# Kernel optimization log

Hardware: AMD Instinct MI355X
Metric: run time of the kernel (lower is better)

Reference implementation:

```python
import jax, jax.numpy as jnp
import numpy as np

MAX_IT = 20
LAMBDA_ROF = 7.0
SIGMA = 1.0 / (7.0 * 0.01)
TAU = 0.01
THETA = 0.5

H, W_DIM = 4096, 4096


def forward_weighted_gradient(x, w):
    # x: (1,H,W), w: (2,H,W) -> (2,H,W)
    x0 = x[0]
    gh = jnp.pad(x0[:, 1:] - x0[:, :-1], ((0, 0), (0, 1)))   # grad[0,:, :-1]
    gv = jnp.pad(x0[1:, :] - x0[:-1, :], ((0, 1), (0, 0)))   # grad[1,:-1,:]
    return jnp.stack([gh, gv], axis=0) * w


def backward_divergence(y):
    # y: (2,H,W) -> (1,H,W)
    yh, yv = y[0], y[1]
    d_h = jnp.concatenate(
        [yh[:, :1], yh[:, 1:-1] - yh[:, :-2], -yh[:, -2:-1]], axis=1)
    d_v = jnp.concatenate(
        [yv[:1, :], yv[1:-1, :] - yv[:-2, :], -yv[-2:-1, :]], axis=0)
    return (d_h + d_v)[None]


def prox_linf_ball(p, r):
    # p - detach(max(p-r,0) - max(-p-r,0))  (clamp treated as data in torch code)
    shrink = jnp.maximum(p - r, 0.0) - jnp.maximum(-p - r, 0.0)
    return p - jax.lax.stop_gradient(shrink)


def setup_inputs() -> dict:
    key = jax.random.key(0)
    k1, _ = jax.random.split(key)
    img_obs = jax.random.uniform(k1, (1, H, W_DIM), dtype=jnp.float32)
    w = jnp.ones((2, H, W_DIM), dtype=jnp.float32)
    return {"img_obs": img_obs, "w": w}


def reference(img_obs, w):
    x0 = img_obs
    x_tilde0 = img_obs
    y0 = jnp.zeros((2,) + img_obs.shape[1:], dtype=img_obs.dtype)

    def step(carry, _):
        x, x_tilde, y = carry
        y = y + SIGMA * forward_weighted_gradient(x_tilde, w)
        y = prox_linf_ball(y, 1.0)
        x_old = x
        x = (x + TAU * backward_divergence(y)
             + LAMBDA_ROF * TAU * img_obs) / (1.0 + LAMBDA_ROF * TAU)
        x_tilde = x + THETA * (x - x_old)
        return (x, x_tilde, y), None

    (x, x_tilde, y), _ = jax.lax.scan(step, (x0, x_tilde0, y0), None, length=MAX_IT)
    return x_tilde
```

## Files before the change

kernel.cpp:

```cpp
#include <hip/hip_runtime.h>

static constexpr int H = 4096;
static constexpr int W = 4096;
static constexpr long N = (long)H * W;

static constexpr int TILE = 64;
static constexpr int HOFF = 12;
static constexpr int R    = TILE + 2*HOFF;
static constexpr int S    = R;
static constexpr int PS   = R * S;
static constexpr int CPR  = R / 8;
static constexpr int NCH  = R * CPR;
static constexpr int NT   = 512;

static constexpr float SIGMA = 14.285714285714286f;
static constexpr float INVD  = 1.0f / 1.07f;
static constexpr float TIV   = 0.01f / 1.07f;
static constexpr float CF    = 0.07f / 1.07f;

typedef _Float16 half8  __attribute__((ext_vector_type(8)));
typedef _Float16 half4v __attribute__((ext_vector_type(4)));

__device__ __forceinline__ half8 splat8(float f) {
    _Float16 h = (_Float16)f;
    half8 v = {h, h, h, h, h, h, h, h};
    return v;
}
__device__ __forceinline__ half8 clamp8(half8 v) {
    v = __builtin_elementwise_min(v, splat8(1.0f));
    v = __builtin_elementwise_max(v, splat8(-1.0f));
    return v;
}

__global__ __launch_bounds__(256) void pack_w(
    const float* __restrict__ wg, _Float16* __restrict__ whp, _Float16* __restrict__ wvp)
{
    const long p = ((long)blockIdx.x * 256 + threadIdx.x) * 8;
    const int i = (int)(p >> 12);
    const float4* hp = reinterpret_cast<const float4*>(wg + p);
    float4 a = hp[0], b = hp[1];
    const float4* vp = reinterpret_cast<const float4*>(wg + N + p);
    float4 c = vp[0], d = vp[1];
    half8 wh, wv;
    wh[0]=(_Float16)(SIGMA*a.x); wh[1]=(_Float16)(SIGMA*a.y);
    wh[2]=(_Float16)(SIGMA*a.z); wh[3]=(_Float16)(SIGMA*a.w);
    wh[4]=(_Float16)(SIGMA*b.x); wh[5]=(_Float16)(SIGMA*b.y);
    wh[6]=(_Float16)(SIGMA*b.z); wh[7]=(_Float16)(SIGMA*b.w);
    wv[0]=(_Float16)(SIGMA*c.x); wv[1]=(_Float16)(SIGMA*c.y);
    wv[2]=(_Float16)(SIGMA*c.z); wv[3]=(_Float16)(SIGMA*c.w);
    wv[4]=(_Float16)(SIGMA*d.x); wv[5]=(_Float16)(SIGMA*d.y);
    wv[6]=(_Float16)(SIGMA*d.z); wv[7]=(_Float16)(SIGMA*d.w);
    if ((p & 4095) + 8 == W) wh[7] = (_Float16)0.0f;
    if (i == H - 1) wv = splat8(0.0f);
    *reinterpret_cast<half8*>(whp + p) = wh;
    *reinterpret_cast<half8*>(wvp + p) = wv;
}

template<int PHASE>
__global__ __launch_bounds__(NT, 4) void fused_pd(
    const float* __restrict__ img,
    const _Float16* __restrict__ whp, const _Float16* __restrict__ wvp,
    _Float16* __restrict__ xg, _Float16* __restrict__ yhg, _Float16* __restrict__ yvg,
    float* __restrict__ out)
{
    __shared__ _Float16 lds_s[2 * PS + NCH + 2];
    _Float16* __restrict__ xtp = lds_s;
    _Float16* __restrict__ yvp = lds_s + PS;
    _Float16* __restrict__ yhe = lds_s + 2 * PS;

    const int tid = threadIdx.x;
    const int gi0 = blockIdx.y * TILE - HOFF;
    const int gj0 = blockIdx.x * TILE - HOFF;
    const bool interior = (gi0 >= 0) && (gj0 >= 0) && (gi0 + R <= H) && (gj0 + R <= W);

    const int t0 = tid, t1 = tid + NT;
    const int i0_ = t0 / CPR, i1_ = t1 / CPR;
    const int b0 = i0_ * S + (t0 - i0_ * CPR) * 8;
    const int b1 = i1_ * S + (t1 - i1_ * CPR) * 8;
    const bool act1 = (t1 < NCH);

    const half8 kTIV  = splat8(TIV);
    const half8 kINVD = splat8(INVD);
    const half8 k15   = splat8(1.5f);
    const half8 kM05  = splat8(-0.5f);

    half8 wh0, wh1, wv0, wv1;
    half8 ci0, ci1;
    half8 x0, x1;
    half8 xt0r, xt1r;
    half8 yh0, yh1, yv0, yv1;

    auto loadC = [&](int t, half8& whr, half8& wvr, half8& cir, half8& xr,
                     half8& xtr, half8& yhr, half8& yvr) {
        const int i  = t / CPR;
        const int j0 = (t - i * CPR) * 8;
        const int gi = gi0 + i;
        const int gj = gj0 + j0;
        if (interior) {
            const long o = (long)gi * W + gj;
            const float4* ip = reinterpret_cast<const float4*>(img + o);
            float4 a = ip[0], b = ip[1];
            float im[8] = {a.x, a.y, a.z, a.w, b.x, b.y, b.z, b.w};
            whr = *reinterpret_cast<const half8*>(whp + o);
            wvr = *reinterpret_cast<const half8*>(wvp + o);
#pragma unroll
            for (int k = 0; k < 8; ++k) cir[k] = (_Float16)(CF * im[k]);
            if (PHASE == 0) {
#pragma unroll
                for (int k = 0; k < 8; ++k) xr[k] = (_Float16)im[k];
                xtr = xr;
                yhr = splat8(0.f); yvr = splat8(0.f);
            } else {
                xr  = *reinterpret_cast<const half8*>(xg  + o);
                yhr = *reinterpret_cast<const half8*>(yhg + o);
                yvr = *reinterpret_cast<const half8*>(yvg + o);
            }
        } else {
            const int gic = min(max(gi, 0), H - 1);
            const bool rowin = (gi >= 0) && (gi < H);
#pragma unroll
            for (int k = 0; k < 8; ++k) {
                const int gjk = gj + k;
                const int gjc = min(max(gjk, 0), W - 1);
                const bool inim = rowin && (gjk >= 0) && (gjk < W);
                const long o = (long)gic * W + gjc;
                const float imf = img[o];
                whr[k] = inim ? whp[o] : (_Float16)0.0f;
                wvr[k] = inim ? wvp[o] : (_Float16)0.0f;
                cir[k] = (_Float16)(CF * imf);
                if (PHASE == 0) {
                    xr[k]  = (_Float16)imf;
                    xtr[k] = (_Float16)imf;
                    yhr[k] = (_Float16)0.0f;
                    yvr[k] = (_Float16)0.0f;
                } else {
                    xr[k]  = xg[o];
                    yhr[k] = inim ? yhg[o] : (_Float16)0.0f;
                    yvr[k] = inim ? yvg[o] : (_Float16)0.0f;
                }
            }
        }
        const int base = i * S + j0;
        if (PHASE == 0) {
            *reinterpret_cast<half8*>(xtp + base) = xtr;
        } else {
            *reinterpret_cast<half8*>(xtp + base) = xr;
            *reinterpret_cast<half8*>(yvp + base) = yvr;
            yhe[t + 1] = yhr[7];
        }
    };
    loadC(t0, wh0, wv0, ci0, x0, xt0r, yh0, yv0);
    if (act1) loadC(t1, wh1, wv1, ci1, x1, xt1r, yh1, yv1);
    if (tid == 0) yhe[0] = (_Float16)0.0f;
    __syncthreads();

    auto dual_all = [&](bool write_yhe) {
        _Float16 rt0 = xtp[b0 + 8];
        half8 bv0 = *reinterpret_cast<const half8*>(xtp + b0 + S);
        _Float16 rt1 = (_Float16)0.f; half8 bv1;
        if (act1) {
            rt1 = xtp[b1 + 8];
            bv1 = *reinterpret_cast<const half8*>(xtp + b1 + S);
        }
        {
            half8 sh = __builtin_shufflevector(xt0r, xt0r, 1, 2, 3, 4, 5, 6, 7, 7);
            sh[7] = rt0;
            yh0 = clamp8((sh - xt0r) * wh0 + yh0);
            yv0 = clamp8((bv0 - xt0r) * wv0 + yv0);
            *reinterpret_cast<half8*>(yvp + b0) = yv0;
            if (write_yhe) yhe[t0 + 1] = yh0[7];
        }
        if (act1) {
            half8 sh = __builtin_shufflevector(xt1r, xt1r, 1, 2, 3, 4, 5, 6, 7, 7);
            sh[7] = rt1;
            yh1 = clamp8((sh - xt1r) * wh1 + yh1);
            yv1 = clamp8((bv1 - xt1r) * wv1 + yv1);
            *reinterpret_cast<half8*>(yvp + b1) = yv1;
            if (write_yhe) yhe[t1 + 1] = yh1[7];
        }
    };
    auto prim_all = [&]() {
        _Float16 yl0 = yhe[t0];
        half8 yva0 = *reinterpret_cast<const half8*>(yvp + b0 - S);
        _Float16 yl1 = (_Float16)0.f; half8 yva1;
        if (act1) {
            yl1  = yhe[t1];
            yva1 = *reinterpret_cast<const half8*>(yvp + b1 - S);
        }
        {
            half8 ysh = __builtin_shufflevector(yh0, yh0, 0, 0, 1, 2, 3, 4, 5, 6);
            ysh[0] = yl0;
            half8 dv = (yh0 - ysh) + (yv0 - yva0);
            half8 tt = dv * kTIV + ci0;
            half8 xn = x0 * kINVD + tt;
            half8 xt = xn * k15 + x0 * kM05;
            x0 = xn; xt0r = xt;
            *reinterpret_cast<half8*>(xtp + b0) = xt;
        }
        if (act1) {
            half8 ysh = __builtin_shufflevector(yh1, yh1, 0, 0, 1, 2, 3, 4, 5, 6);
            ysh[0] = yl1;
            half8 dv = (yh1 - ysh) + (yv1 - yva1);
            half8 tt = dv * kTIV + ci1;
            half8 xn = x1 * kINVD + tt;
            half8 xt = xn * k15 + x1 * kM05;
            x1 = xn; xt1r = xt;
            *reinterpret_cast<half8*>(xtp + b1) = xt;
        }
    };

    if (PHASE == 1) {
        prim_all();
        __syncthreads();
    }
    const int NIT = (PHASE == 0) ? 10 : 9;
    for (int it = 0; it < NIT; ++it) {
        dual_all(true);
        __syncthreads();
        prim_all();
        __syncthreads();
    }
    if (PHASE == 0) {
        dual_all(false);
        __syncthreads();
    }

    const int r  = tid >> 3;
    const int k  = tid & 7;
    const int lb = (HOFF + r) * S + HOFF + k * 8;
    const long gb = (long)(blockIdx.y * TILE + r) * W + blockIdx.x * TILE + k * 8;

    if (PHASE == 0) {
        {
            half4v a0 = *reinterpret_cast<const half4v*>(yvp + lb);
            half4v a1 = *reinterpret_cast<const half4v*>(yvp + lb + 4);
            half8 o; o[0]=a0[0];o[1]=a0[1];o[2]=a0[2];o[3]=a0[3];
                     o[4]=a1[0];o[5]=a1[1];o[6]=a1[2];o[7]=a1[3];
            *reinterpret_cast<half8*>(yvg + gb) = o;
        }
        __syncthreads();
        *reinterpret_cast<half8*>(xtp + b0) = x0;
        *reinterpret_cast<half8*>(yvp + b0) = yh0;
        if (act1) {
            *reinterpret_cast<half8*>(xtp + b1) = x1;
            *reinterpret_cast<half8*>(yvp + b1) = yh1;
        }
        __syncthreads();
        {
            half4v a0 = *reinterpret_cast<const half4v*>(xtp + lb);
            half4v a1 = *reinterpret_cast<const half4v*>(xtp + lb + 4);
            half8 o; o[0]=a0[0];o[1]=a0[1];o[2]=a0[2];o[3]=a0[3];
                     o[4]=a1[0];o[5]=a1[1];o[6]=a1[2];o[7]=a1[3];
            *reinterpret_cast<half8*>(xg + gb) = o;
            half4v b0v = *reinterpret_cast<const half4v*>(yvp + lb);
            half4v b1v = *reinterpret_cast<const half4v*>(yvp + lb + 4);
            half8 o2; o2[0]=b0v[0];o2[1]=b0v[1];o2[2]=b0v[2];o2[3]=b0v[3];
                      o2[4]=b1v[0];o2[5]=b1v[1];o2[6]=b1v[2];o2[7]=b1v[3];
            *reinterpret_cast<half8*>(yhg + gb) = o2;
        }
    } else {
        half4v a = *reinterpret_cast<const half4v*>(xtp + lb);
        half4v b = *reinterpret_cast<const half4v*>(xtp + lb + 4);
        float4 o0 = make_float4((float)a[0], (float)a[1], (float)a[2], (float)a[3]);
        float4 o1 = make_float4((float)b[0], (float)b[1], (float)b[2], (float)b[3]);
        *reinterpret_cast<float4*>(out + gb)     = o0;
        *reinterpret_cast<float4*>(out + gb + 4) = o1;
    }
}

extern "C" void kernel_launch(void* const* d_in, const int* in_sizes, int n_in,
                              void* d_out, int out_size, void* d_ws, size_t ws_size,
                              hipStream_t stream) {
    const float* img = (const float*)d_in[0];
    const float* wg  = (const float*)d_in[1];
    float* out = (float*)d_out;

    _Float16* ws16 = (_Float16*)d_ws;
    _Float16* whp = ws16;
    _Float16* wvp = ws16 + N;
    _Float16* xg  = ws16 + 2 * N;
    _Float16* yhg = ws16 + 3 * N;
    _Float16* yvg = ws16 + 4 * N;

    pack_w<<<dim3((int)(N / 8 / 256)), dim3(256), 0, stream>>>(wg, whp, wvp);

    dim3 grid(W / TILE, H / TILE);
    fused_pd<0><<<grid, dim3(NT), 0, stream>>>(img, whp, wvp, xg, yhg, yvg, out);
    fused_pd<1><<<grid, dim3(NT), 0, stream>>>(img, whp, wvp, xg, yhg, yvg, out);
}
```

Baseline: 344.6 us.

## Pair rows per thread so vertical neighbours come from registers, shrinking LDS traffic

Each thread now owns two vertically adjacent 8-wide chunks (rows 2p and 2p+1) instead of two chunks far apart. The vertical gradient and divergence between the paired rows are taken directly from registers. Only the even-row xt, odd-row yv, and single boundary halves go through LDS, which halves the shared-memory arrays and the LDS reads and writes per iteration. Final results are written straight from registers to global memory, dropping the extra LDS staging passes and barriers. The cost is more complex indexing, partial-vector edge stores, and some idle threads, since only NTASK of the 512 threads are active.

```diff
diff --git a/kernel.cpp b/kernel.cpp
--- a/kernel.cpp
+++ b/kernel.cpp
@@ -7,10 +7,10 @@
 static constexpr int TILE = 64;
 static constexpr int HOFF = 12;
 static constexpr int R    = TILE + 2*HOFF;
-static constexpr int S    = R;
-static constexpr int PS   = R * S;
 static constexpr int CPR  = R / 8;
-static constexpr int NCH  = R * CPR;
+static constexpr int PR   = R / 2;
+static constexpr int NTASK= PR * CPR;
+static constexpr int PSE  = PR * R;
 static constexpr int NT   = 512;
 
 static constexpr float SIGMA = 14.285714285714286f;
@@ -30,6 +30,12 @@
     v = __builtin_elementwise_min(v, splat8(1.0f));
     v = __builtin_elementwise_max(v, splat8(-1.0f));
     return v;
+}
+__device__ __forceinline__ half4v lo4(half8 v) {
+    half4v r = {v[0], v[1], v[2], v[3]}; return r;
+}
+__device__ __forceinline__ half4v hi4(half8 v) {
+    half4v r = {v[4], v[5], v[6], v[7]}; return r;
 }
 
 __global__ __launch_bounds__(256) void pack_w(
@@ -63,21 +69,22 @@
     _Float16* __restrict__ xg, _Float16* __restrict__ yhg, _Float16* __restrict__ yvg,
     float* __restrict__ out)
 {
-    __shared__ _Float16 lds_s[2 * PS + NCH + 2];
-    _Float16* __restrict__ xtp = lds_s;
-    _Float16* __restrict__ yvp = lds_s + PS;
-    _Float16* __restrict__ yhe = lds_s + 2 * PS;
+    __shared__ _Float16 lds_s[2 * PSE + 3 * (NTASK + 2)];
+    _Float16* __restrict__ xte  = lds_s;
+    _Float16* __restrict__ yvo  = lds_s + PSE;
+    _Float16* __restrict__ yheA = lds_s + 2 * PSE;
+    _Float16* __restrict__ yheB = yheA + (NTASK + 2);
+    _Float16* __restrict__ xteo = yheB + (NTASK + 2);
 
     const int tid = threadIdx.x;
+    const bool act = tid < NTASK;
+    const int t  = act ? tid : 0;
+    const int p  = t / CPR;
+    const int j0 = (t - p * CPR) * 8;
+    const int be = p * R + j0;
     const int gi0 = blockIdx.y * TILE - HOFF;
     const int gj0 = blockIdx.x * TILE - HOFF;
     const bool interior = (gi0 >= 0) && (gj0 >= 0) && (gi0 + R <= H) && (gj0 + R <= W);
-
-    const int t0 = tid, t1 = tid + NT;
-    const int i0_ = t0 / CPR, i1_ = t1 / CPR;
-    const int b0 = i0_ * S + (t0 - i0_ * CPR) * 8;
-    const int b1 = i1_ * S + (t1 - i1_ * CPR) * 8;
-    const bool act1 = (t1 < NCH);
 
     const half8 kTIV  = splat8(TIV);
     const half8 kINVD = splat8(INVD);
@@ -90,12 +97,8 @@
     half8 xt0r, xt1r;
     half8 yh0, yh1, yv0, yv1;
 
-    auto loadC = [&](int t, half8& whr, half8& wvr, half8& cir, half8& xr,
-                     half8& xtr, half8& yhr, half8& yvr) {
-        const int i  = t / CPR;
-        const int j0 = (t - i * CPR) * 8;
-        const int gi = gi0 + i;
-        const int gj = gj0 + j0;
+    auto loadRow = [&](int gi, int gj, half8& whr, half8& wvr, half8& cir,
+                       half8& xr, half8& yhr, half8& yvr) {
         if (interior) {
             const long o = (long)gi * W + gj;
             const float4* ip = reinterpret_cast<const float4*>(img + o);
@@ -108,7 +111,6 @@
             if (PHASE == 0) {
 #pragma unroll
                 for (int k = 0; k < 8; ++k) xr[k] = (_Float16)im[k];
-                xtr = xr;
                 yhr = splat8(0.f); yvr = splat8(0.f);
             } else {
                 xr  = *reinterpret_cast<const half8*>(xg  + o);
@@ -130,7 +132,6 @@
                 cir[k] = (_Float16)(CF * imf);
                 if (PHASE == 0) {
                     xr[k]  = (_Float16)imf;
-                    xtr[k] = (_Float16)imf;
                     yhr[k] = (_Float16)0.0f;
                     yvr[k] = (_Float16)0.0f;
                 } else {
@@ -140,131 +141,138 @@
                 }
             }
         }
-        const int base = i * S + j0;
+    };
+    if (act) {
+        const int gi = gi0 + 2 * p;
+        const int gj = gj0 + j0;
+        loadRow(gi,     gj, wh0, wv0, ci0, x0, yh0, yv0);
+        loadRow(gi + 1, gj, wh1, wv1, ci1, x1, yh1, yv1);
         if (PHASE == 0) {
-            *reinterpret_cast<half8*>(xtp + base) = xtr;
+            xt0r = x0; xt1r = x1;
+            *reinterpret_cast<half8*>(xte + be) = xt0r;
+            *reinterpret_cast<half8*>(yvo + be) = splat8(0.f);
+            xteo[t] = xt1r[0];
+            yheA[1 + t] = (_Float16)0.0f;
+            yheB[1 + t] = (_Float16)0.0f;
         } else {
-            *reinterpret_cast<half8*>(xtp + base) = xr;
-            *reinterpret_cast<half8*>(yvp + base) = yvr;
-            yhe[t + 1] = yhr[7];
+            *reinterpret_cast<half8*>(yvo + be) = yv1;
+            yheA[1 + t] = yh0[7];
+            yheB[1 + t] = yh1[7];
+        }
+    }
+    if (tid == NT - 1) {
+        yheA[0] = (_Float16)0.0f;
+        yheB[0] = (_Float16)0.0f;
+        xteo[NTASK]     = (_Float16)0.0f;
+        xteo[NTASK + 1] = (_Float16)0.0f;
+    }
+    __syncthreads();
+
+    auto dual_all = [&](bool writes) {
+        if (act) {
+            _Float16 rt0 = xte[be + 8];
+            _Float16 rt1 = xteo[t + 1];
+            half8 bv1 = *reinterpret_cast<const half8*>(xte + be + R);
+            half8 sh0 = __builtin_shufflevector(xt0r, xt0r, 1, 2, 3, 4, 5, 6, 7, 7);
+            sh0[7] = rt0;
+            half8 sh1 = __builtin_shufflevector(xt1r, xt1r, 1, 2, 3, 4, 5, 6, 7, 7);
+            sh1[7] = rt1;
+            yh0 = clamp8((sh0 - xt0r) * wh0 + yh0);
+            yv0 = clamp8((xt1r - xt0r) * wv0 + yv0);
+            yh1 = clamp8((sh1 - xt1r) * wh1 + yh1);
+            yv1 = clamp8((bv1 - xt1r) * wv1 + yv1);
+            if (writes) {
+                *reinterpret_cast<half8*>(yvo + be) = yv1;
+                yheA[1 + t] = yh0[7];
+                yheB[1 + t] = yh1[7];
+            }
         }
     };
-    loadC(t0, wh0, wv0, ci0, x0, xt0r, yh0, yv0);
-    if (act1) loadC(t1, wh1, wv1, ci1, x1, xt1r, yh1, yv1);
-    if (tid == 0) yhe[0] = (_Float16)0.0f;
-    __syncthreads();
-
-    auto dual_all = [&](bool write_yhe) {
-        _Float16 rt0 = xtp[b0 + 8];
-        half8 bv0 = *reinterpret_cast<const half8*>(xtp + b0 + S);
-        _Float16 rt1 = (_Float16)0.f; half8 bv1;
-        if (act1) {
-            rt1 = xtp[b1 + 8];
-            bv1 = *reinterpret_cast<const half8*>(xtp + b1 + S);
-        }
-        {
-            half8 sh = __builtin_shufflevector(xt0r, xt0r, 1, 2, 3, 4, 5, 6, 7, 7);
-            sh[7] = rt0;
-            yh0 = clamp8((sh - xt0r) * wh0 + yh0);
-            yv0 = clamp8((bv0 - xt0r) * wv0 + yv0);
-            *reinterpret_cast<half8*>(yvp + b0) = yv0;
-            if (write_yhe) yhe[t0 + 1] = yh0[7];
-        }
-        if (act1) {
-            half8 sh = __builtin_shufflevector(xt1r, xt1r, 1, 2, 3, 4, 5, 6, 7, 7);
-            sh[7] = rt1;
-            yh1 = clamp8((sh - xt1r) * wh1 + yh1);
-            yv1 = clamp8((bv1 - xt1r) * wv1 + yv1);
-            *reinterpret_cast<half8*>(yvp + b1) = yv1;
-            if (write_yhe) yhe[t1 + 1] = yh1[7];
+    auto prim_all = [&](bool writes) {
+        if (act) {
+            _Float16 yl0 = yheA[t];
+            _Float16 yl1 = yheB[t];
+            half8 yva0 = *reinterpret_cast<const half8*>(yvo + be - R);
+            half8 ysh0 = __builtin_shufflevector(yh0, yh0, 0, 0, 1, 2, 3, 4, 5, 6);
+            ysh0[0] = yl0;
+            half8 ysh1 = __builtin_shufflevector(yh1, yh1, 0, 0, 1, 2, 3, 4, 5, 6);
+            ysh1[0] = yl1;
+            half8 dv0 = (yh0 - ysh0) + (yv0 - yva0);
+            half8 dv1 = (yh1 - ysh1) + (yv1 - yv0);
+            half8 tt0 = dv0 * kTIV + ci0;
+            half8 xn0 = x0 * kINVD + tt0;
+            half8 xtn0 = xn0 * k15 + x0 * kM05;
+            x0 = xn0; xt0r = xtn0;
+            half8 tt1 = dv1 * kTIV + ci1;
+            half8 xn1 = x1 * kINVD + tt1;
+            half8 xtn1 = xn1 * k15 + x1 * kM05;
+            x1 = xn1; xt1r = xtn1;
+            if (writes) {
+                *reinterpret_cast<half8*>(xte + be) = xt0r;
+                xteo[t] = xt1r[0];
+            }
         }
     };
-    auto prim_all = [&]() {
-        _Float16 yl0 = yhe[t0];
-        half8 yva0 = *reinterpret_cast<const half8*>(yvp + b0 - S);
-        _Float16 yl1 = (_Float16)0.f; half8 yva1;
-        if (act1) {
-            yl1  = yhe[t1];
-            yva1 = *reinterpret_cast<const half8*>(yvp + b1 - S);
-        }
-        {
-            half8 ysh = __builtin_shufflevector(yh0, yh0, 0, 0, 1, 2, 3, 4, 5, 6);
-            ysh[0] = yl0;
-            half8 dv = (yh0 - ysh) + (yv0 - yva0);
-            half8 tt = dv * kTIV + ci0;
-            half8 xn = x0 * kINVD + tt;
-            half8 xt = xn * k15 + x0 * kM05;
-            x0 = xn; xt0r = xt;
-            *reinterpret_cast<half8*>(xtp + b0) = xt;
-        }
-        if (act1) {
-            half8 ysh = __builtin_shufflevector(yh1, yh1, 0, 0, 1, 2, 3, 4, 5, 6);
-            ysh[0] = yl1;
-            half8 dv = (yh1 - ysh) + (yv1 - yva1);
-            half8 tt = dv * kTIV + ci1;
-            half8 xn = x1 * kINVD + tt;
-            half8 xt = xn * k15 + x1 * kM05;
-            x1 = xn; xt1r = xt;
-            *reinterpret_cast<half8*>(xtp + b1) = xt;
-        }
-    };
 
     if (PHASE == 1) {
-        prim_all();
+        prim_all(true);
         __syncthreads();
     }
     const int NIT = (PHASE == 0) ? 10 : 9;
     for (int it = 0; it < NIT; ++it) {
         dual_all(true);
         __syncthreads();
-        prim_all();
+        prim_all(!(PHASE == 1 && it == NIT - 1));
         __syncthreads();
     }
     if (PHASE == 0) {
         dual_all(false);
-        __syncthreads();
-    }
-
-    const int r  = tid >> 3;
-    const int k  = tid & 7;
-    const int lb = (HOFF + r) * S + HOFF + k * 8;
-    const long gb = (long)(blockIdx.y * TILE + r) * W + blockIdx.x * TILE + k * 8;
-
-    if (PHASE == 0) {
-        {
-            half4v a0 = *reinterpret_cast<const half4v*>(yvp + lb);
-            half4v a1 = *reinterpret_cast<const half4v*>(yvp + lb + 4);
-            half8 o; o[0]=a0[0];o[1]=a0[1];o[2]=a0[2];o[3]=a0[3];
-                     o[4]=a1[0];o[5]=a1[1];o[6]=a1[2];o[7]=a1[3];
-            *reinterpret_cast<half8*>(yvg + gb) = o;
-        }
-        __syncthreads();
-        *reinterpret_cast<half8*>(xtp + b0) = x0;
-        *reinterpret_cast<half8*>(yvp + b0) = yh0;
-        if (act1) {
-            *reinterpret_cast<half8*>(xtp + b1) = x1;
-            *reinterpret_cast<half8*>(yvp + b1) = yh1;
-        }
-        __syncthreads();
-        {
-            half4v a0 = *reinterpret_cast<const half4v*>(xtp + lb);
-            half4v a1 = *reinterpret_cast<const half4v*>(xtp + lb + 4);
-            half8 o; o[0]=a0[0];o[1]=a0[1];o[2]=a0[2];o[3]=a0[3];
-                     o[4]=a1[0];o[5]=a1[1];o[6]=a1[2];o[7]=a1[3];
-            *reinterpret_cast<half8*>(xg + gb) = o;
-            half4v b0v = *reinterpret_cast<const half4v*>(yvp + lb);
-            half4v b1v = *reinterpret_cast<const half4v*>(yvp + lb + 4);
-            half8 o2; o2[0]=b0v[0];o2[1]=b0v[1];o2[2]=b0v[2];o2[3]=b0v[3];
-                      o2[4]=b1v[0];o2[5]=b1v[1];o2[6]=b1v[2];o2[7]=b1v[3];
-            *reinterpret_cast<half8*>(yhg + gb) = o2;
-        }
-    } else {
-        half4v a = *reinterpret_cast<const half4v*>(xtp + lb);
-        half4v b = *reinterpret_cast<const half4v*>(xtp + lb + 4);
-        float4 o0 = make_float4((float)a[0], (float)a[1], (float)a[2], (float)a[3]);
-        float4 o1 = make_float4((float)b[0], (float)b[1], (float)b[2], (float)b[3]);
-        *reinterpret_cast<float4*>(out + gb)     = o0;
-        *reinterpret_cast<float4*>(out + gb + 4) = o1;
+    }
+
+    if (act && p >= 6 && p < 38 && j0 >= 8 && j0 <= 72) {
+        const long g0 = (long)(gi0 + 2 * p) * W + (gj0 + j0);
+        const long g1 = g0 + W;
+        if (PHASE == 0) {
+            if (j0 >= 16 && j0 <= 64) {
+                *reinterpret_cast<half8*>(xg  + g0) = x0;
+                *reinterpret_cast<half8*>(xg  + g1) = x1;
+                *reinterpret_cast<half8*>(yhg + g0) = yh0;
+                *reinterpret_cast<half8*>(yhg + g1) = yh1;
+                *reinterpret_cast<half8*>(yvg + g0) = yv0;
+                *reinterpret_cast<half8*>(yvg + g1) = yv1;
+            } else if (j0 == 8) {
+                *reinterpret_cast<half4v*>(xg  + g0 + 4) = hi4(x0);
+                *reinterpret_cast<half4v*>(xg  + g1 + 4) = hi4(x1);
+                *reinterpret_cast<half4v*>(yhg + g0 + 4) = hi4(yh0);
+                *reinterpret_cast<half4v*>(yhg + g1 + 4) = hi4(yh1);
+                *reinterpret_cast<half4v*>(yvg + g0 + 4) = hi4(yv0);
+                *reinterpret_cast<half4v*>(yvg + g1 + 4) = hi4(yv1);
+            } else {
+                *reinterpret_cast<half4v*>(xg  + g0) = lo4(x0);
+                *reinterpret_cast<half4v*>(xg  + g1) = lo4(x1);
+                *reinterpret_cast<half4v*>(yhg + g0) = lo4(yh0);
+                *reinterpret_cast<half4v*>(yhg + g1) = lo4(yh1);
+                *reinterpret_cast<half4v*>(yvg + g0) = lo4(yv0);
+                *reinterpret_cast<half4v*>(yvg + g1) = lo4(yv1);
+            }
+        } else {
+            float4 a0 = make_float4((float)xt0r[0], (float)xt0r[1], (float)xt0r[2], (float)xt0r[3]);
+            float4 a1 = make_float4((float)xt0r[4], (float)xt0r[5], (float)xt0r[6], (float)xt0r[7]);
+            float4 b0 = make_float4((float)xt1r[0], (float)xt1r[1], (float)xt1r[2], (float)xt1r[3]);
+            float4 b1 = make_float4((float)xt1r[4], (float)xt1r[5], (float)xt1r[6], (float)xt1r[7]);
+            if (j0 >= 16 && j0 <= 64) {
+                *reinterpret_cast<float4*>(out + g0)     = a0;
+                *reinterpret_cast<float4*>(out + g0 + 4) = a1;
+                *reinterpret_cast<float4*>(out + g1)     = b0;
+                *reinterpret_cast<float4*>(out + g1 + 4) = b1;
+            } else if (j0 == 8) {
+                *reinterpret_cast<float4*>(out + g0 + 4) = a1;
+                *reinterpret_cast<float4*>(out + g1 + 4) = b1;
+            } else {
+                *reinterpret_cast<float4*>(out + g0) = a0;
+                *reinterpret_cast<float4*>(out + g1) = b0;
+            }
+        }
     }
 }
 
```

New measurement: 342.3 us. No clear change (-0.7%).
